# Kernel optimization log

Hardware: AMD Instinct MI355X
Metric: run time of the kernel (lower is better)

Reference implementation:

```python
import jax, jax.numpy as jnp
import numpy as np

N, DIM, H, DH = 2048, 1024, 16, 64
LARGE_NEG = -1e10
LN_EPS = 1e-6  # flax LayerNorm default


def setup_inputs() -> dict:
    key = jax.random.key(0)
    ks = jax.random.split(key, 6)
    x = jax.random.normal(ks[0], (N, DIM), dtype=jnp.float32)
    pos_sin = jax.random.uniform(ks[1], (N - 1, DH // 2), dtype=jnp.float32)
    pos_cos = jax.random.uniform(ks[2], (N - 1, DH // 2), dtype=jnp.float32)
    mask = jax.random.bernoulli(ks[3], 0.9, (N - 1,))
    ln_scale = jnp.ones((DIM,), jnp.float32)
    ln_bias = jnp.zeros((DIM,), jnp.float32)
    w_qkv = jax.random.normal(ks[4], (DIM, 3 * H * DH), jnp.float32) * (DIM ** -0.5)
    w_out = jax.random.normal(ks[5], (H * DH, DIM), jnp.float32) * ((H * DH) ** -0.5)
    b_out = jnp.zeros((DIM,), jnp.float32)
    return {"x": x, "pos_sin": pos_sin, "pos_cos": pos_cos, "mask": mask,
            "ln_scale": ln_scale, "ln_bias": ln_bias,
            "w_qkv": w_qkv, "w_out": w_out, "b_out": b_out}


def _rotate_every_two(t):
    # t: [i, h, d] -> pairwise rotation along d
    x1 = t[:, :, ::2]
    x2 = t[:, :, 1::2]
    return jnp.stack((-x2, x1), axis=-1).reshape(t.shape)


def _apply_rope(t, sin, cos):
    # sin/cos: [i, d/2] -> interleave-repeat to [i, 1, d] (einops 'b n -> b (n j)', j=2)
    sin2 = jnp.repeat(sin, 2, axis=-1)[:, None, :]
    cos2 = jnp.repeat(cos, 2, axis=-1)[:, None, :]
    return t * cos2 + _rotate_every_two(t) * sin2


def reference(x, pos_sin, pos_cos, mask, ln_scale, ln_bias, w_qkv, w_out, b_out):
    n, dim_in = x.shape
    scale = dim_in ** -0.5  # NOTE: full model dim, as in the source

    # LayerNorm over last axis
    mu = jnp.mean(x, axis=-1, keepdims=True)
    var = jnp.mean(jnp.square(x - mu), axis=-1, keepdims=True)
    xn = (x - mu) * jax.lax.rsqrt(var + LN_EPS) * ln_scale + ln_bias

    # QKV projection (no bias)
    qkv = xn @ w_qkv  # [n, 3*h*d]
    q, k, v = jnp.split(qkv, 3, axis=-1)
    q, k, v = (t.reshape(n, H, DH) for t in (q, k, v))

    # Selective RoPE: rotate all positions except the first token
    q = q.at[1:].set(_apply_rope(q[1:], pos_sin, pos_cos))
    k = k.at[1:].set(_apply_rope(k[1:], pos_sin, pos_cos))

    # Head-last similarity [i, j, h]
    sim = jnp.einsum('ihd,jhd->ijh', q, k) * scale

    # Padding mask: prepend True for position 0, broadcast as (1, j, 1)
    pad_mask = jnp.pad(mask, (1, 0), constant_values=True)[None, :, None]

    # Causal mask: triu of an (n-1)x(n-1) block padded with False on row/col 0
    tri = jnp.pad(jnp.ones((n - 1, n - 1), bool), ((1, 0), (1, 0)), constant_values=False)
    causal_mask = jnp.triu(tri, 1)[:, :, None]  # k = j - i + 1 = 1
    full_mask = (~causal_mask) & pad_mask

    sim = jnp.where(full_mask, sim, LARGE_NEG)
    attn = jax.nn.softmax(sim, axis=-2)  # softmax over j (non-last axis)

    out = jnp.einsum('ijh,jhd->ihd', attn, v).reshape(n, H * DH)
    return out @ w_out + b_out
```

## Files before the change

### kernel.cpp

```cpp
#include <hip/hip_runtime.h>
#include <hip/hip_bf16.h>
#include <stdint.h>

typedef __bf16 bf16_t;
typedef __bf16 bf16x8 __attribute__((ext_vector_type(8)));
typedef __bf16 bf16x4 __attribute__((ext_vector_type(4)));
typedef float  f32x4  __attribute__((ext_vector_type(4)));

#define DEV __device__ __forceinline__

static constexpr int NTOK = 2048;
static constexpr int DIM  = 1024;
static constexpr int NH   = 16;
static constexpr int DH   = 64;
static constexpr int QKVN = 3072;
static constexpr int SLOTS_PER_HEAD = 40;
static constexpr int PART_SLOTS = 36;
static constexpr int PART_STRIDE = 17408;
static constexpr float L2E = 1.44269504f;

DEV void gload_lds16(const void* g, void* l) {
  __builtin_amdgcn_global_load_lds(
      (__attribute__((address_space(1))) void*)(g),
      (__attribute__((address_space(3))) void*)(l), 16, 0, 0);
}

DEV float bf2f(bf16_t b) { return (float)b; }

__global__ __launch_bounds__(256) void k_ln_tc(const float* __restrict__ x,
                                               const float* __restrict__ gamma,
                                               const float* __restrict__ beta,
                                               bf16_t* __restrict__ xn,
                                               const float* __restrict__ wsrc,
                                               bf16_t* __restrict__ wdst,
                                               const float* __restrict__ wosrc,
                                               bf16_t* __restrict__ wodst) {
  __shared__ float tile[64][65];
  __shared__ float red[8];
  int b = blockIdx.x;
  if (b < NTOK) {
    const int row = b;
    const int t = threadIdx.x;
    const float4* x4 = reinterpret_cast<const float4*>(x);
    float4 v = x4[(size_t)row * 256 + t];
    float s  = v.x + v.y + v.z + v.w;
    float s2 = v.x * v.x + v.y * v.y + v.z * v.z + v.w * v.w;
#pragma unroll
    for (int o = 1; o < 64; o <<= 1) {
      s  += __shfl_xor(s, o, 64);
      s2 += __shfl_xor(s2, o, 64);
    }
    const int w = t >> 6, lane = t & 63;
    if (lane == 0) { red[w] = s; red[4 + w] = s2; }
    __syncthreads();
    s  = red[0] + red[1] + red[2] + red[3];
    s2 = red[4] + red[5] + red[6] + red[7];
    const float mu  = s * (1.0f / 1024.0f);
    const float var = s2 * (1.0f / 1024.0f) - mu * mu;
    const float inv = rsqrtf(var + 1e-6f);
    const float4 g = reinterpret_cast<const float4*>(gamma)[t];
    const float4 bb = reinterpret_cast<const float4*>(beta)[t];
    bf16x4 o;
    o[0] = (bf16_t)((v.x - mu) * inv * g.x + bb.x);
    o[1] = (bf16_t)((v.y - mu) * inv * g.y + bb.y);
    o[2] = (bf16_t)((v.z - mu) * inv * g.z + bb.z);
    o[3] = (bf16_t)((v.w - mu) * inv * g.w + bb.w);
    *reinterpret_cast<bf16x4*>(xn + (size_t)row * DIM + t * 4) = o;
  } else if (b < NTOK + 768) {
    b -= NTOK;
    const int c0 = (b % 48) * 64;
    const int r0 = (b / 48) * 64;
    const int tx = threadIdx.x & 63;
    const int ty = threadIdx.x >> 6;
#pragma unroll
    for (int i = 0; i < 16; ++i) {
      int r = ty + i * 4;
      tile[r][tx] = wsrc[(size_t)(r0 + r) * 3072 + c0 + tx];
    }
    __syncthreads();
#pragma unroll
    for (int i = 0; i < 16; ++i) {
      int r = ty + i * 4;
      wdst[(size_t)(c0 + r) * 1024 + r0 + tx] = (bf16_t)tile[tx][r];
    }
  } else {
    b -= (NTOK + 768);
    const int c0 = (b & 15) * 64;
    const int r0 = (b >> 4) * 64;
    const int tx = threadIdx.x & 63;
    const int ty = threadIdx.x >> 6;
#pragma unroll
    for (int i = 0; i < 16; ++i) {
      int r = ty + i * 4;
      tile[r][tx] = wosrc[(size_t)(r0 + r) * 1024 + c0 + tx];
    }
    __syncthreads();
#pragma unroll
    for (int i = 0; i < 16; ++i) {
      int r = ty + i * 4;
      wodst[(size_t)(c0 + r) * 1024 + r0 + tx] = (bf16_t)tile[tx][r];
    }
  }
}

__global__ __launch_bounds__(256) void k_gemm_qkv(const bf16_t* __restrict__ A,
                                                  const bf16_t* __restrict__ Bt,
                                                  bf16_t* __restrict__ qkv,
                                                  bf16_t* __restrict__ Vt,
                                                  const float* __restrict__ psin,
                                                  const float* __restrict__ pcos) {
  __shared__ alignas(16) bf16_t As[2][64 * 32];
  __shared__ alignas(16) bf16_t Bs[2][128 * 32];
  const int K = DIM;
  const int tid = threadIdx.x, lane = tid & 63, w = tid >> 6;
  const int bm = blockIdx.x * 64, bn = blockIdx.y * 128;
  const int wr = (w >> 1) * 32, wc = (w & 1) * 64;
  f32x4 acc[2][4];
#pragma unroll
  for (int i = 0; i < 2; ++i)
#pragma unroll
    for (int j = 0; j < 4; ++j) acc[i][j] = f32x4{0.f, 0.f, 0.f, 0.f};

  const int srow  = lane >> 2;
  const int scol8 = (lane & 3) * 8;

#define GSTAGEQ(KT, BUF)                                                              \
  {                                                                                   \
    _Pragma("unroll") for (int it = 0; it < 3; ++it) {                                \
      int s = w * 3 + it;                                                             \
      if (s < 4)                                                                      \
        gload_lds16(A + (size_t)(bm + s * 16 + srow) * K + (KT) + scol8,              \
                    (char*)As + (BUF) * 4096 + s * 1024 + lane * 16);                 \
      else                                                                            \
        gload_lds16(Bt + (size_t)(bn + (s - 4) * 16 + srow) * K + (KT) + scol8,       \
                    (char*)Bs + (BUF) * 8192 + (s - 4) * 1024 + lane * 16);           \
    }                                                                                 \
  }

  GSTAGEQ(0, 0)
  int buf = 0;
  for (int kt = 0; kt < K; kt += 32, buf ^= 1) {
    if (kt + 32 < K) {
      GSTAGEQ(kt + 32, buf ^ 1)
      asm volatile("s_waitcnt vmcnt(3)" ::: "memory");
    } else {
      asm volatile("s_waitcnt vmcnt(0)" ::: "memory");
    }
    __builtin_amdgcn_s_barrier();
    bf16x8 af[2], bfr[4];
#pragma unroll
    for (int i = 0; i < 2; ++i) {
      int mrow = wr + i * 16 + (lane & 15);
      af[i] = *reinterpret_cast<const bf16x8*>((const char*)As + buf * 4096 + mrow * 64 +
                                               (lane >> 4) * 16);
    }
#pragma unroll
    for (int j = 0; j < 4; ++j) {
      int nrow = wc + j * 16 + (lane & 15);
      bfr[j] = *reinterpret_cast<const bf16x8*>((const char*)Bs + buf * 8192 + nrow * 64 +
                                                (lane >> 4) * 16);
    }
#pragma unroll
    for (int i = 0; i < 2; ++i)
#pragma unroll
      for (int j = 0; j < 4; ++j)
        acc[i][j] = __builtin_amdgcn_mfma_f32_16x16x32_bf16(af[i], bfr[j], acc[i][j], 0, 0, 0);
    __builtin_amdgcn_s_barrier();
  }
#undef GSTAGEQ

  if (bn >= 2048) {
#pragma unroll
    for (int i = 0; i < 2; ++i)
#pragma unroll
      for (int j = 0; j < 4; ++j) {
        int d = bn - 2048 + wc + j * 16 + (lane & 15);
        int n0v = bm + wr + i * 16 + (lane >> 4) * 4;
        bf16x4 v4;
#pragma unroll
        for (int r = 0; r < 4; ++r) v4[r] = (bf16_t)acc[i][j][r];
        *reinterpret_cast<bf16x4*>(Vt + (size_t)d * NTOK + n0v) = v4;
      }
  } else {
#pragma unroll
    for (int i = 0; i < 2; ++i)
#pragma unroll
      for (int j = 0; j < 4; ++j) {
        int nn = bn + wc + j * 16 + (lane & 15);
        int tt = (nn & 63) >> 1;
        bool isq = nn < 1024;
#pragma unroll
        for (int r = 0; r < 4; ++r) {
          int mm = bm + wr + i * 16 + (lane >> 4) * 4 + r;
          float v = acc[i][j][r];
          float p = __shfl_xor(v, 1, 64);
          int pidx = (mm >= 1 ? mm - 1 : 0) * 32 + tt;
          float sn = psin[pidx], cs = pcos[pidx];
          float roped = (nn & 1) ? (v * cs + p * sn) : (v * cs - p * sn);
          if (mm < 1) roped = v;
          if (isq && mm >= 1) roped *= 0.03125f;
          qkv[(size_t)mm * QKVN + nn] = (bf16_t)roped;
        }
      }
  }
}

template <int F32OUT>
__global__ __launch_bounds__(256) void k_gemm64(const bf16_t* __restrict__ A,
                                                const bf16_t* __restrict__ Bt,
                                                bf16_t* __restrict__ Cb,
                                                float* __restrict__ Cf,
                                                const float* __restrict__ bias,
                                                int M, int N, int K) {
  __shared__ alignas(16) bf16_t As[2][64 * 32];
  __shared__ alignas(16) bf16_t Bs[2][128 * 32];
  const int tid = threadIdx.x, lane = tid & 63, w = tid >> 6;
  const int bm = blockIdx.x * 64, bn = blockIdx.y * 128;
  const int wr = (w >> 1) * 32, wc = (w & 1) * 64;
  f32x4 acc[2][4];
#pragma unroll
  for (int i = 0; i < 2; ++i)
#pragma unroll
    for (int j = 0; j < 4; ++j) acc[i][j] = f32x4{0.f, 0.f, 0.f, 0.f};

  const int srow  = lane >> 2;
  const int scol8 = (lane & 3) * 8;

#define GSTAGE64(KT, BUF)                                                             \
  {                                                                                   \
    _Pragma("unroll") for (int it = 0; it < 3; ++it) {                                \
      int s = w * 3 + it;                                                             \
      if (s < 4)                                                                      \
        gload_lds16(A + (size_t)(bm + s * 16 + srow) * K + (KT) + scol8,              \
                    (char*)As + (BUF) * 4096 + s * 1024 + lane * 16);                 \
      else                                                                            \
        gload_lds16(Bt + (size_t)(bn + (s - 4) * 16 + srow) * K + (KT) + scol8,       \
                    (char*)Bs + (BUF) * 8192 + (s - 4) * 1024 + lane * 16);           \
    }                                                                                 \
  }

  GSTAGE64(0, 0)
  int buf = 0;
  for (int kt = 0; kt < K; kt += 32, buf ^= 1) {
    if (kt + 32 < K) {
      GSTAGE64(kt + 32, buf ^ 1)
      asm volatile("s_waitcnt vmcnt(3)" ::: "memory");
    } else {
      asm volatile("s_waitcnt vmcnt(0)" ::: "memory");
    }
    __builtin_amdgcn_s_barrier();
    bf16x8 af[2], bfr[4];
#pragma unroll
    for (int i = 0; i < 2; ++i) {
      int mrow = wr + i * 16 + (lane & 15);
      af[i] = *reinterpret_cast<const bf16x8*>((const char*)As + buf * 4096 + mrow * 64 +
                                               (lane >> 4) * 16);
    }
#pragma unroll
    for (int j = 0; j < 4; ++j) {
      int nrow = wc + j * 16 + (lane & 15);
      bfr[j] = *reinterpret_cast<const bf16x8*>((const char*)Bs + buf * 8192 + nrow * 64 +
                                                (lane >> 4) * 16);
    }
#pragma unroll
    for (int i = 0; i < 2; ++i)
#pragma unroll
      for (int j = 0; j < 4; ++j)
        acc[i][j] = __builtin_amdgcn_mfma_f32_16x16x32_bf16(af[i], bfr[j], acc[i][j], 0, 0, 0);
    __builtin_amdgcn_s_barrier();
  }
#undef GSTAGE64

#pragma unroll
  for (int i = 0; i < 2; ++i)
#pragma unroll
    for (int j = 0; j < 4; ++j)
#pragma unroll
      for (int r = 0; r < 4; ++r) {
        int mm = bm + wr + i * 16 + (lane >> 4) * 4 + r;
        int nn = bn + wc + j * 16 + (lane & 15);
        float val = acc[i][j][r];
        if (F32OUT)
          Cf[(size_t)mm * N + nn] = val + bias[nn];
        else
          Cb[(size_t)mm * N + nn] = (bf16_t)val;
      }
}

__global__ __launch_bounds__(512) void k_attn_part(const bf16_t* __restrict__ qkv,
                                                   const bf16_t* __restrict__ Vt,
                                                   const int* __restrict__ mask,
                                                   char* __restrict__ part,
                                                   bf16_t* __restrict__ Ob) {
  __shared__ alignas(16) bf16_t Ks[2][64][64];
  __shared__ alignas(16) bf16_t Vs[2][64][64];
  __shared__ alignas(16) float padf[512];

  const int h = blockIdx.y;

  if (blockIdx.x == SLOTS_PER_HEAD) {
    float* qv   = padf;
    float* sbuf = (float*)Ks;
    float* red  = (float*)Vs;
    float* red2 = (float*)Vs + 64;
    const int t = threadIdx.x, lane = t & 63, w8 = t >> 6;
    if (t < 64) qv[t] = (float)qkv[h * DH + t];
    __syncthreads();
    float sm[4];
    float lmax = -1e30f;
#pragma unroll
    for (int p = 0; p < 4; ++p) {
      int j = p * 512 + t;
      const bf16_t* kr = qkv + (size_t)j * QKVN + DIM + h * DH;
      float s = 0.f;
#pragma unroll
      for (int u = 0; u < 8; ++u) {
        bf16x8 kv8 = *reinterpret_cast<const bf16x8*>(kr + u * 8);
#pragma unroll
        for (int e = 0; e < 8; ++e) s += qv[u * 8 + e] * (float)kv8[e];
      }
      bool padj = (j == 0) || (mask[j - 1] != 0);
      s = padj ? s * 0.03125f : -1e30f;
      sm[p] = s;
      lmax = fmaxf(lmax, s);
    }
#pragma unroll
    for (int o = 1; o < 64; o <<= 1) lmax = fmaxf(lmax, __shfl_xor(lmax, o, 64));
    if (lane == 0) red[w8] = lmax;
    __syncthreads();
    float M = red[0];
#pragma unroll
    for (int i = 1; i < 8; ++i) M = fmaxf(M, red[i]);
    __syncthreads();
    float ls = 0.f;
#pragma unroll
    for (int p = 0; p < 4; ++p) {
      float pe = __expf(sm[p] - M);
      sbuf[p * 512 + t] = pe;
      ls += pe;
    }
#pragma unroll
    for (int o = 1; o < 64; o <<= 1) ls += __shfl_xor(ls, o, 64);
    if (lane == 0) red[w8] = ls;
    __syncthreads();
    float L = red[0];
#pragma unroll
    for (int i = 1; i < 8; ++i) L += red[i];

    const int d = t & 63, qr = t >> 6;
    const bf16_t* vr = Vt + ((size_t)h * DH + d) * NTOK + qr * 256;
    float a = 0.f;
#pragma unroll 8
    for (int u = 0; u < 32; ++u) {
      bf16x8 v8 = *reinterpret_cast<const bf16x8*>(vr + u * 8);
#pragma unroll
      for (int e = 0; e < 8; ++e) a += sbuf[qr * 256 + u * 8 + e] * (float)v8[e];
    }
    red2[qr * 64 + d] = a;
    __syncthreads();
    if (t < 64) {
      float o = 0.f;
#pragma unroll
      for (int i = 0; i < 8; ++i) o += red2[i * 64 + t];
      Ob[h * DH + t] = (bf16_t)(o / L);
    }
    return;
  }

  const int slot = (SLOTS_PER_HEAD - 1) - blockIdx.x;
  int gq;
  if (slot < 4) gq = 0; else if (slot < 12) gq = 1; else if (slot < 24) gq = 2; else gq = 3;
  const int tt = slot - 2 * gq * (gq + 1);
  const int Q = (gq << 2) + tt / (gq + 1);
  const int c2 = tt - (tt / (gq + 1)) * (gq + 1);
  const int q0 = Q * 128;
  const int kbeg = c2 * 512;
  const int kvlen = (Q + 1) * 128;
  const int klen = min(512, kvlen - kbeg);
  const int ntiles = klen >> 6;
  const int nch = gq + 1;

  const int tid = threadIdx.x, lane = tid & 63, w = tid >> 6;
  const int g = lane >> 4;
  const int c = lane & 15;

  for (int jr = tid; jr < klen; jr += 512) {
    int j = kbeg + jr;
    padf[jr] = (j == 0 || mask[j - 1] != 0) ? 1.f : 0.f;
  }

  const int iw = q0 + w * 16;
  bf16x8 qf[2];
  {
    const bf16_t* qp = qkv + (size_t)(iw + c) * QKVN + h * DH + g * 8;
    qf[0] = *reinterpret_cast<const bf16x8*>(qp);
    qf[1] = *reinterpret_cast<const bf16x8*>(qp + 32);
  }
  bf16x8 ones;
#pragma unroll
  for (int e = 0; e < 8; ++e) ones[e] = (bf16_t)1.0f;

  float m_run = -1e30f, m2 = -1e30f;
  f32x4 acc[4], accl;
#pragma unroll
  for (int df = 0; df < 4; ++df) acc[df] = f32x4{0.f, 0.f, 0.f, 0.f};
  accl = f32x4{0.f, 0.f, 0.f, 0.f};

  const int r8 = lane >> 3;

#define STAGE(KB, BUF)                                                                   \
  {                                                                                      \
    _Pragma("unroll") for (int i2 = 0; i2 < 2; ++i2) {                                   \
      int s = w * 2 + i2;                                                                \
      int sw = (lane & 7) ^ r8 ^ ((s & 3) << 1);                                         \
      if (s < 8) {                                                                       \
        int row = s * 8 + r8;                                                            \
        gload_lds16(qkv + (size_t)((KB) + row) * QKVN + DIM + h * DH + sw * 8,           \
                    (char*)Ks + (BUF)*8192 + s * 1024 + lane * 16);                      \
      } else {                                                                           \
        int row = (s - 8) * 8 + r8;                                                      \
        gload_lds16(Vt + ((size_t)h * DH + row) * NTOK + (KB) + sw * 8,                  \
                    (char*)Vs + (BUF)*8192 + (s - 8) * 1024 + lane * 16);                \
      }                                                                                  \
    }                                                                                    \
  }

  STAGE(kbeg, 0)

  for (int it = 0; it < ntiles; ++it) {
    const int buf = it & 1;
    if (it + 1 < ntiles) {
      STAGE(kbeg + (it + 1) * 64, buf ^ 1)
      asm volatile("s_waitcnt vmcnt(2)" ::: "memory");
    } else {
      asm volatile("s_waitcnt vmcnt(0)" ::: "memory");
    }
    __builtin_amdgcn_s_barrier();

    const int k0 = kbeg + it * 64;
    if (k0 <= iw + 15) {
      const char* KsT = (const char*)Ks + buf * 8192;
      const char* VsT = (const char*)Vs + buf * 8192;

      f32x4 sfr[4];
      __builtin_amdgcn_s_setprio(1);
#pragma unroll
      for (int f = 0; f < 4; ++f) {
        int key7 = ((f & 1) * 4) | (c & 3);
        int key = (f >> 1) * 32 + (c >> 2) * 8 + key7;
        int phi = key7 ^ (((c >> 2) & 3) << 1);
        f32x4 s = f32x4{0.f, 0.f, 0.f, 0.f};
#pragma unroll
        for (int kd = 0; kd < 2; ++kd) {
          bf16x8 kf = *reinterpret_cast<const bf16x8*>(
              KsT + key * 128 + (((kd * 4 + g) ^ phi) << 4));
          s = __builtin_amdgcn_mfma_f32_16x16x32_bf16(kf, qf[kd], s, 0, 0, 0);
        }
        sfr[f] = s;
      }
      __builtin_amdgcn_s_setprio(0);

      float pm = fmaxf(fmaxf(sfr[0][0], sfr[0][1]), fmaxf(sfr[0][2], sfr[0][3]));
#pragma unroll
      for (int f = 1; f < 4; ++f)
        pm = fmaxf(pm, fmaxf(fmaxf(sfr[f][0], sfr[f][1]), fmaxf(sfr[f][2], sfr[f][3])));
      pm = fmaxf(pm, __shfl_xor(pm, 16, 64));
      pm = fmaxf(pm, __shfl_xor(pm, 32, 64));

      if (!__all(pm <= m_run + 8.f)) {
        float mnew = fmaxf(m_run, pm);
        float corr = __builtin_amdgcn_exp2f((m_run - mnew) * L2E);
        m_run = mnew;
        m2 = mnew * L2E;
#pragma unroll
        for (int r = 0; r < 4; ++r) {
          float cr = __shfl(corr, g * 4 + r, 64);
          accl[r] *= cr;
#pragma unroll
          for (int df = 0; df < 4; ++df) acc[df][r] *= cr;
        }
      }

      const bool needC = (k0 + 63 > iw);
      const int qlane = iw + c;
      bf16x8 pa[2];
#pragma unroll
      for (int f = 0; f < 4; ++f) {
        int jb = (k0 - kbeg) + (f >> 1) * 32 + g * 8 + (f & 1) * 4;
        f32x4 pad4 = *reinterpret_cast<const f32x4*>(padf + jb);
#pragma unroll
        for (int r = 0; r < 4; ++r) {
          float pe = __builtin_amdgcn_exp2f(__builtin_fmaf(sfr[f][r], L2E, -m2)) * pad4[r];
          if (needC) pe = (kbeg + jb + r <= qlane) ? pe : 0.f;
          pa[f >> 1][(f & 1) * 4 + r] = (bf16_t)pe;
        }
      }

      __builtin_amdgcn_s_setprio(1);
#pragma unroll
      for (int ks = 0; ks < 2; ++ks) {
        accl = __builtin_amdgcn_mfma_f32_16x16x32_bf16(pa[ks], ones, accl, 0, 0, 0);
#pragma unroll
        for (int df = 0; df < 4; ++df) {
          int d = df * 16 + c;
          int phv = (d & 7) ^ (((d >> 3) & 3) << 1);
          bf16x8 vf = *reinterpret_cast<const bf16x8*>(
              VsT + d * 128 + (((ks * 4 + g) ^ phv) << 4));
          acc[df] = __builtin_amdgcn_mfma_f32_16x16x32_bf16(pa[ks], vf, acc[df], 0, 0, 0);
        }
      }
      __builtin_amdgcn_s_setprio(0);
    }
    __builtin_amdgcn_s_barrier();
  }
#undef STAGE

  if (nch == 1) {
#pragma unroll
    for (int r = 0; r < 4; ++r) {
      float inv = 1.0f / accl[r];
      int row = w * 16 + g * 4 + r;
#pragma unroll
      for (int df = 0; df < 4; ++df) {
        if (q0 + row != 0)
          Ob[(size_t)(q0 + row) * DIM + h * DH + df * 16 + c] = (bf16_t)(acc[df][r] * inv);
      }
    }
    return;
  }

  char* pb = part + (size_t)(h * PART_SLOTS + (slot - 4)) * PART_STRIDE;
  bf16_t* po = (bf16_t*)pb;
  float* pmo = (float*)(pb + 16384);
  float* plo = (float*)(pb + 16896);
  float mq[4];
#pragma unroll
  for (int r = 0; r < 4; ++r) mq[r] = __shfl(m2, g * 4 + r, 64);
#pragma unroll
  for (int df = 0; df < 4; ++df)
#pragma unroll
    for (int r = 0; r < 4; ++r) {
      int row = w * 16 + g * 4 + r;
      po[row * 64 + df * 16 + c] = (bf16_t)acc[df][r];
    }
  if (c == 0) {
#pragma unroll
    for (int r = 0; r < 4; ++r) {
      int row = w * 16 + g * 4 + r;
      pmo[row] = mq[r];
      plo[row] = accl[r];
    }
  }
}

__global__ __launch_bounds__(256) void k_merge(const char* __restrict__ part,
                                               bf16_t* __restrict__ Ob) {
  const int Q = blockIdx.x + 4, h = blockIdx.y;
  const int g = Q >> 2, nch = g + 1;
  const int cum = 2 * g * (g + 1) + (Q & 3) * nch - 4;
  const int t = threadIdx.x;
  const int row = t >> 1, half = t & 1;

  float acc[32];
#pragma unroll
  for (int e = 0; e < 32; ++e) acc[e] = 0.f;
  float M = -3e38f, L = 0.f;

  for (int c = 0; c < nch; ++c) {
    const char* pb = part + (size_t)(h * PART_SLOTS + cum + c) * PART_STRIDE;
    float mc = ((const float*)(pb + 16384))[row];
    float lc = ((const float*)(pb + 16896))[row];
    float Mn = fmaxf(M, mc);
    float sOld = __builtin_amdgcn_exp2f(M - Mn), sNew = __builtin_amdgcn_exp2f(mc - Mn);
    M = Mn;
    L = L * sOld + lc * sNew;
    const bf16_t* od = (const bf16_t*)pb + row * 64 + half * 32;
#pragma unroll
    for (int e4 = 0; e4 < 4; ++e4) {
      bf16x8 o8 = *reinterpret_cast<const bf16x8*>(od + e4 * 8);
#pragma unroll
      for (int e = 0; e < 8; ++e)
        acc[e4 * 8 + e] = acc[e4 * 8 + e] * sOld + (float)o8[e] * sNew;
    }
  }
  const float inv = 1.0f / L;
  bf16_t* dst = Ob + (size_t)(Q * 128 + row) * DIM + h * DH + half * 32;
#pragma unroll
  for (int e4 = 0; e4 < 4; ++e4) {
    bf16x8 r8o;
#pragma unroll
    for (int e = 0; e < 8; ++e) r8o[e] = (bf16_t)(acc[e4 * 8 + e] * inv);
    *reinterpret_cast<bf16x8*>(dst + e4 * 8) = r8o;
  }
}

extern "C" void kernel_launch(void* const* d_in, const int* in_sizes, int n_in,
                              void* d_out, int out_size, void* d_ws, size_t ws_size,
                              hipStream_t stream) {
  const float* x       = (const float*)d_in[0];
  const float* pos_sin = (const float*)d_in[1];
  const float* pos_cos = (const float*)d_in[2];
  const int*   mask    = (const int*)d_in[3];
  const float* ln_s    = (const float*)d_in[4];
  const float* ln_b    = (const float*)d_in[5];
  const float* w_qkv   = (const float*)d_in[6];
  const float* w_out   = (const float*)d_in[7];
  const float* b_out   = (const float*)d_in[8];
  float* out = (float*)d_out;

  if (ws_size < 33554432u) return;

  char* ws = (char*)d_ws;
  bf16_t* qkv  = (bf16_t*)(ws + 0);
  bf16_t* Vt   = (bf16_t*)(ws + 12582912);
  bf16_t* Ob   = (bf16_t*)(ws + 16777216);
  bf16_t* Wot  = (bf16_t*)(ws + 20971520);
  bf16_t* xn   = (bf16_t*)(ws + 23068672);
  bf16_t* Wqt  = (bf16_t*)(ws + 27262976);
  char*   part = ws + 23068672;

  k_ln_tc<<<NTOK + 768 + 256, 256, 0, stream>>>(x, ln_s, ln_b, xn, w_qkv, Wqt, w_out, Wot);
  k_gemm_qkv<<<dim3(32, 24), 256, 0, stream>>>(xn, Wqt, qkv, Vt, pos_sin, pos_cos);
  k_attn_part<<<dim3(SLOTS_PER_HEAD + 1, NH), 512, 0, stream>>>(qkv, Vt, mask, part, Ob);
  k_merge<<<dim3(12, 16), 256, 0, stream>>>(part, Ob);
  k_gemm64<1><<<dim3(32, 8), 256, 0, stream>>>(Ob, Wot, nullptr, out, b_out,
                                               NTOK, DIM, DIM);
}
```

Baseline: 96.82 us.

## Enlarge QKV GEMM tile and give each attention wave two query strips

```diff
diff --git a/kernel.cpp b/kernel.cpp
--- a/kernel.cpp
+++ b/kernel.cpp
@@ -109,15 +109,15 @@
                                                   bf16_t* __restrict__ Vt,
                                                   const float* __restrict__ psin,
                                                   const float* __restrict__ pcos) {
-  __shared__ alignas(16) bf16_t As[2][64 * 32];
+  __shared__ alignas(16) bf16_t As[2][128 * 32];
   __shared__ alignas(16) bf16_t Bs[2][128 * 32];
   const int K = DIM;
   const int tid = threadIdx.x, lane = tid & 63, w = tid >> 6;
-  const int bm = blockIdx.x * 64, bn = blockIdx.y * 128;
-  const int wr = (w >> 1) * 32, wc = (w & 1) * 64;
-  f32x4 acc[2][4];
-#pragma unroll
-  for (int i = 0; i < 2; ++i)
+  const int bm = blockIdx.x * 128, bn = blockIdx.y * 128;
+  const int wr = (w >> 1) * 64, wc = (w & 1) * 64;
+  f32x4 acc[4][4];
+#pragma unroll
+  for (int i = 0; i < 4; ++i)
 #pragma unroll
     for (int j = 0; j < 4; ++j) acc[i][j] = f32x4{0.f, 0.f, 0.f, 0.f};
 
@@ -126,14 +126,12 @@
 
 #define GSTAGEQ(KT, BUF)                                                              \
   {                                                                                   \
-    _Pragma("unroll") for (int it = 0; it < 3; ++it) {                                \
-      int s = w * 3 + it;                                                             \
-      if (s < 4)                                                                      \
-        gload_lds16(A + (size_t)(bm + s * 16 + srow) * K + (KT) + scol8,              \
-                    (char*)As + (BUF) * 4096 + s * 1024 + lane * 16);                 \
-      else                                                                            \
-        gload_lds16(Bt + (size_t)(bn + (s - 4) * 16 + srow) * K + (KT) + scol8,       \
-                    (char*)Bs + (BUF) * 8192 + (s - 4) * 1024 + lane * 16);           \
+    _Pragma("unroll") for (int it = 0; it < 2; ++it) {                                \
+      int seg = w * 2 + it;                                                           \
+      gload_lds16(A  + (size_t)(bm + seg * 16 + srow) * K + (KT) + scol8,             \
+                  (char*)As + (BUF) * 8192 + seg * 1024 + lane * 16);                 \
+      gload_lds16(Bt + (size_t)(bn + seg * 16 + srow) * K + (KT) + scol8,             \
+                  (char*)Bs + (BUF) * 8192 + seg * 1024 + lane * 16);                 \
     }                                                                                 \
   }
 
@@ -142,16 +140,16 @@
   for (int kt = 0; kt < K; kt += 32, buf ^= 1) {
     if (kt + 32 < K) {
       GSTAGEQ(kt + 32, buf ^ 1)
-      asm volatile("s_waitcnt vmcnt(3)" ::: "memory");
+      asm volatile("s_waitcnt vmcnt(4)" ::: "memory");
     } else {
       asm volatile("s_waitcnt vmcnt(0)" ::: "memory");
     }
     __builtin_amdgcn_s_barrier();
-    bf16x8 af[2], bfr[4];
-#pragma unroll
-    for (int i = 0; i < 2; ++i) {
+    bf16x8 af[4], bfr[4];
+#pragma unroll
+    for (int i = 0; i < 4; ++i) {
       int mrow = wr + i * 16 + (lane & 15);
-      af[i] = *reinterpret_cast<const bf16x8*>((const char*)As + buf * 4096 + mrow * 64 +
+      af[i] = *reinterpret_cast<const bf16x8*>((const char*)As + buf * 8192 + mrow * 64 +
                                                (lane >> 4) * 16);
     }
 #pragma unroll
@@ -161,7 +159,7 @@
                                                 (lane >> 4) * 16);
     }
 #pragma unroll
-    for (int i = 0; i < 2; ++i)
+    for (int i = 0; i < 4; ++i)
 #pragma unroll
       for (int j = 0; j < 4; ++j)
         acc[i][j] = __builtin_amdgcn_mfma_f32_16x16x32_bf16(af[i], bfr[j], acc[i][j], 0, 0, 0);
@@ -171,7 +169,7 @@
 
   if (bn >= 2048) {
 #pragma unroll
-    for (int i = 0; i < 2; ++i)
+    for (int i = 0; i < 4; ++i)
 #pragma unroll
       for (int j = 0; j < 4; ++j) {
         int d = bn - 2048 + wc + j * 16 + (lane & 15);
@@ -183,7 +181,7 @@
       }
   } else {
 #pragma unroll
-    for (int i = 0; i < 2; ++i)
+    for (int i = 0; i < 4; ++i)
 #pragma unroll
       for (int j = 0; j < 4; ++j) {
         int nn = bn + wc + j * 16 + (lane & 15);
@@ -287,7 +285,7 @@
       }
 }
 
-__global__ __launch_bounds__(512) void k_attn_part(const bf16_t* __restrict__ qkv,
+__global__ __launch_bounds__(256) void k_attn_part(const bf16_t* __restrict__ qkv,
                                                    const bf16_t* __restrict__ Vt,
                                                    const int* __restrict__ mask,
                                                    char* __restrict__ part,
@@ -303,14 +301,14 @@
     float* sbuf = (float*)Ks;
     float* red  = (float*)Vs;
     float* red2 = (float*)Vs + 64;
-    const int t = threadIdx.x, lane = t & 63, w8 = t >> 6;
+    const int t = threadIdx.x, lane = t & 63, w4 = t >> 6;
     if (t < 64) qv[t] = (float)qkv[h * DH + t];
     __syncthreads();
-    float sm[4];
+    float sm[8];
     float lmax = -1e30f;
 #pragma unroll
-    for (int p = 0; p < 4; ++p) {
-      int j = p * 512 + t;
+    for (int p = 0; p < 8; ++p) {
+      int j = p * 256 + t;
       const bf16_t* kr = qkv + (size_t)j * QKVN + DIM + h * DH;
       float s = 0.f;
 #pragma unroll
@@ -326,42 +324,37 @@
     }
 #pragma unroll
     for (int o = 1; o < 64; o <<= 1) lmax = fmaxf(lmax, __shfl_xor(lmax, o, 64));
-    if (lane == 0) red[w8] = lmax;
-    __syncthreads();
-    float M = red[0];
-#pragma unroll
-    for (int i = 1; i < 8; ++i) M = fmaxf(M, red[i]);
+    if (lane == 0) red[w4] = lmax;
+    __syncthreads();
+    const float M = fmaxf(fmaxf(red[0], red[1]), fmaxf(red[2], red[3]));
     __syncthreads();
     float ls = 0.f;
 #pragma unroll
-    for (int p = 0; p < 4; ++p) {
+    for (int p = 0; p < 8; ++p) {
       float pe = __expf(sm[p] - M);
-      sbuf[p * 512 + t] = pe;
+      sbuf[p * 256 + t] = pe;
       ls += pe;
     }
 #pragma unroll
     for (int o = 1; o < 64; o <<= 1) ls += __shfl_xor(ls, o, 64);
-    if (lane == 0) red[w8] = ls;
-    __syncthreads();
-    float L = red[0];
-#pragma unroll
-    for (int i = 1; i < 8; ++i) L += red[i];
+    __syncthreads();
+    if (lane == 0) red[w4] = ls;
+    __syncthreads();
+    const float L = red[0] + red[1] + red[2] + red[3];
 
     const int d = t & 63, qr = t >> 6;
-    const bf16_t* vr = Vt + ((size_t)h * DH + d) * NTOK + qr * 256;
+    const bf16_t* vr = Vt + ((size_t)h * DH + d) * NTOK + qr * 512;
     float a = 0.f;
 #pragma unroll 8
-    for (int u = 0; u < 32; ++u) {
+    for (int u = 0; u < 64; ++u) {
       bf16x8 v8 = *reinterpret_cast<const bf16x8*>(vr + u * 8);
 #pragma unroll
-      for (int e = 0; e < 8; ++e) a += sbuf[qr * 256 + u * 8 + e] * (float)v8[e];
+      for (int e = 0; e < 8; ++e) a += sbuf[qr * 512 + u * 8 + e] * (float)v8[e];
     }
     red2[qr * 64 + d] = a;
     __syncthreads();
     if (t < 64) {
-      float o = 0.f;
-#pragma unroll
-      for (int i = 0; i < 8; ++i) o += red2[i * 64 + t];
+      float o = red2[t] + red2[64 + t] + red2[128 + t] + red2[192 + t];
       Ob[h * DH + t] = (bf16_t)(o / L);
     }
     return;
@@ -384,34 +377,38 @@
   const int g = lane >> 4;
   const int c = lane & 15;
 
-  for (int jr = tid; jr < klen; jr += 512) {
+  for (int jr = tid; jr < klen; jr += 256) {
     int j = kbeg + jr;
     padf[jr] = (j == 0 || mask[j - 1] != 0) ? 1.f : 0.f;
   }
 
-  const int iw = q0 + w * 16;
-  bf16x8 qf[2];
-  {
-    const bf16_t* qp = qkv + (size_t)(iw + c) * QKVN + h * DH + g * 8;
-    qf[0] = *reinterpret_cast<const bf16x8*>(qp);
-    qf[1] = *reinterpret_cast<const bf16x8*>(qp + 32);
+  const int iw = q0 + w * 32;
+  bf16x8 qf[2][2];
+#pragma unroll
+  for (int qh = 0; qh < 2; ++qh) {
+    const bf16_t* qp = qkv + (size_t)(iw + qh * 16 + c) * QKVN + h * DH + g * 8;
+    qf[qh][0] = *reinterpret_cast<const bf16x8*>(qp);
+    qf[qh][1] = *reinterpret_cast<const bf16x8*>(qp + 32);
   }
   bf16x8 ones;
 #pragma unroll
   for (int e = 0; e < 8; ++e) ones[e] = (bf16_t)1.0f;
 
-  float m_run = -1e30f, m2 = -1e30f;
-  f32x4 acc[4], accl;
-#pragma unroll
-  for (int df = 0; df < 4; ++df) acc[df] = f32x4{0.f, 0.f, 0.f, 0.f};
-  accl = f32x4{0.f, 0.f, 0.f, 0.f};
+  float m_run[2] = {-1e30f, -1e30f}, m2_[2] = {-1e30f, -1e30f};
+  f32x4 acc[2][4], accl[2];
+#pragma unroll
+  for (int qh = 0; qh < 2; ++qh) {
+    accl[qh] = f32x4{0.f, 0.f, 0.f, 0.f};
+#pragma unroll
+    for (int df = 0; df < 4; ++df) acc[qh][df] = f32x4{0.f, 0.f, 0.f, 0.f};
+  }
 
   const int r8 = lane >> 3;
 
 #define STAGE(KB, BUF)                                                                   \
   {                                                                                      \
-    _Pragma("unroll") for (int i2 = 0; i2 < 2; ++i2) {                                   \
-      int s = w * 2 + i2;                                                                \
+    _Pragma("unroll") for (int i2 = 0; i2 < 4; ++i2) {                                   \
+      int s = w * 4 + i2;                                                                \
       int sw = (lane & 7) ^ r8 ^ ((s & 3) << 1);                                         \
       if (s < 8) {                                                                       \
         int row = s * 8 + r8;                                                            \
@@ -431,82 +428,104 @@
     const int buf = it & 1;
     if (it + 1 < ntiles) {
       STAGE(kbeg + (it + 1) * 64, buf ^ 1)
-      asm volatile("s_waitcnt vmcnt(2)" ::: "memory");
+      asm volatile("s_waitcnt vmcnt(4)" ::: "memory");
     } else {
       asm volatile("s_waitcnt vmcnt(0)" ::: "memory");
     }
     __builtin_amdgcn_s_barrier();
 
     const int k0 = kbeg + it * 64;
-    if (k0 <= iw + 15) {
+    if (k0 <= iw + 31) {
       const char* KsT = (const char*)Ks + buf * 8192;
       const char* VsT = (const char*)Vs + buf * 8192;
 
-      f32x4 sfr[4];
+      f32x4 sfr[2][4];
       __builtin_amdgcn_s_setprio(1);
 #pragma unroll
       for (int f = 0; f < 4; ++f) {
         int key7 = ((f & 1) * 4) | (c & 3);
         int key = (f >> 1) * 32 + (c >> 2) * 8 + key7;
         int phi = key7 ^ (((c >> 2) & 3) << 1);
-        f32x4 s = f32x4{0.f, 0.f, 0.f, 0.f};
+        f32x4 s0 = f32x4{0.f, 0.f, 0.f, 0.f};
+        f32x4 s1 = f32x4{0.f, 0.f, 0.f, 0.f};
 #pragma unroll
         for (int kd = 0; kd < 2; ++kd) {
           bf16x8 kf = *reinterpret_cast<const bf16x8*>(
               KsT + key * 128 + (((kd * 4 + g) ^ phi) << 4));
-          s = __builtin_amdgcn_mfma_f32_16x16x32_bf16(kf, qf[kd], s, 0, 0, 0);
+          s0 = __builtin_amdgcn_mfma_f32_16x16x32_bf16(kf, qf[0][kd], s0, 0, 0, 0);
+          s1 = __builtin_amdgcn_mfma_f32_16x16x32_bf16(kf, qf[1][kd], s1, 0, 0, 0);
         }
-        sfr[f] = s;
+        sfr[0][f] = s0;
+        sfr[1][f] = s1;
       }
       __builtin_amdgcn_s_setprio(0);
 
-      float pm = fmaxf(fmaxf(sfr[0][0], sfr[0][1]), fmaxf(sfr[0][2], sfr[0][3]));
-#pragma unroll
-      for (int f = 1; f < 4; ++f)
-        pm = fmaxf(pm, fmaxf(fmaxf(sfr[f][0], sfr[f][1]), fmaxf(sfr[f][2], sfr[f][3])));
-      pm = fmaxf(pm, __shfl_xor(pm, 16, 64));
-      pm = fmaxf(pm, __shfl_xor(pm, 32, 64));
-
-      if (!__all(pm <= m_run + 8.f)) {
-        float mnew = fmaxf(m_run, pm);
-        float corr = __builtin_amdgcn_exp2f((m_run - mnew) * L2E);
-        m_run = mnew;
-        m2 = mnew * L2E;
-#pragma unroll
-        for (int r = 0; r < 4; ++r) {
-          float cr = __shfl(corr, g * 4 + r, 64);
-          accl[r] *= cr;
-#pragma unroll
-          for (int df = 0; df < 4; ++df) acc[df][r] *= cr;
+      float pm[2];
+#pragma unroll
+      for (int qh = 0; qh < 2; ++qh) {
+        float p = fmaxf(fmaxf(sfr[qh][0][0], sfr[qh][0][1]),
+                        fmaxf(sfr[qh][0][2], sfr[qh][0][3]));
+#pragma unroll
+        for (int f = 1; f < 4; ++f)
+          p = fmaxf(p, fmaxf(fmaxf(sfr[qh][f][0], sfr[qh][f][1]),
+                             fmaxf(sfr[qh][f][2], sfr[qh][f][3])));
+        p = fmaxf(p, __shfl_xor(p, 16, 64));
+        p = fmaxf(p, __shfl_xor(p, 32, 64));
+        pm[qh] = p;
+      }
+
+      int dok = (pm[0] <= m_run[0] + 8.f) && (pm[1] <= m_run[1] + 8.f);
+      if (!__all(dok)) {
+#pragma unroll
+        for (int qh = 0; qh < 2; ++qh) {
+          float mnew = fmaxf(m_run[qh], pm[qh]);
+          float corr = __builtin_amdgcn_exp2f((m_run[qh] - mnew) * L2E);
+          m_run[qh] = mnew;
+          m2_[qh] = mnew * L2E;
+#pragma unroll
+          for (int r = 0; r < 4; ++r) {
+            float cr = __shfl(corr, g * 4 + r, 64);
+            accl[qh][r] *= cr;
+#pragma unroll
+            for (int df = 0; df < 4; ++df) acc[qh][df][r] *= cr;
+          }
         }
       }
 
-      const bool needC = (k0 + 63 > iw);
-      const int qlane = iw + c;
-      bf16x8 pa[2];
-#pragma unroll
-      for (int f = 0; f < 4; ++f) {
-        int jb = (k0 - kbeg) + (f >> 1) * 32 + g * 8 + (f & 1) * 4;
-        f32x4 pad4 = *reinterpret_cast<const f32x4*>(padf + jb);
-#pragma unroll
-        for (int r = 0; r < 4; ++r) {
-          float pe = __builtin_amdgcn_exp2f(__builtin_fmaf(sfr[f][r], L2E, -m2)) * pad4[r];
-          if (needC) pe = (kbeg + jb + r <= qlane) ? pe : 0.f;
-          pa[f >> 1][(f & 1) * 4 + r] = (bf16_t)pe;
+      bf16x8 pa[2][2];
+#pragma unroll
+      for (int qh = 0; qh < 2; ++qh) {
+        const bool needC = (k0 + 63 > iw + qh * 16);
+        const int qlane = iw + qh * 16 + c;
+#pragma unroll
+        for (int f = 0; f < 4; ++f) {
+          int jb = (k0 - kbeg) + (f >> 1) * 32 + g * 8 + (f & 1) * 4;
+          f32x4 pad4 = *reinterpret_cast<const f32x4*>(padf + jb);
+#pragma unroll
+          for (int r = 0; r < 4; ++r) {
+            float pe = __builtin_amdgcn_exp2f(__builtin_fmaf(sfr[qh][f][r], L2E, -m2_[qh])) *
+                       pad4[r];
+            if (needC) pe = (kbeg + jb + r <= qlane) ? pe : 0.f;
+            pa[qh][f >> 1][(f & 1) * 4 + r] = (bf16_t)pe;
+          }
         }
       }
 
       __builtin_amdgcn_s_setprio(1);
 #pragma unroll
       for (int ks = 0; ks < 2; ++ks) {
-        accl = __builtin_amdgcn_mfma_f32_16x16x32_bf16(pa[ks], ones, accl, 0, 0, 0);
+        accl[0] = __builtin_amdgcn_mfma_f32_16x16x32_bf16(pa[0][ks], ones, accl[0], 0, 0, 0);
+        accl[1] = __builtin_amdgcn_mfma_f32_16x16x32_bf16(pa[1][ks], ones, accl[1], 0, 0, 0);
 #pragma unroll
         for (int df = 0; df < 4; ++df) {
           int d = df * 16 + c;
           int phv = (d & 7) ^ (((d >> 3) & 3) << 1);
           bf16x8 vf = *reinterpret_cast<const bf16x8*>(
               VsT + d * 128 + (((ks * 4 + g) ^ phv) << 4));
-          acc[df] = __builtin_amdgcn_mfma_f32_16x16x32_bf16(pa[ks], vf, acc[df], 0, 0, 0);
+          acc[0][df] = __builtin_amdgcn_mfma_f32_16x16x32_bf16(pa[0][ks], vf, acc[0][df],
+                                                               0, 0, 0);
+          acc[1][df] = __builtin_amdgcn_mfma_f32_16x16x32_bf16(pa[1][ks], vf, acc[1][df],
+                                                               0, 0, 0);
         }
       }
       __builtin_amdgcn_s_setprio(0);
@@ -517,15 +536,18 @@
 
   if (nch == 1) {
 #pragma unroll
-    for (int r = 0; r < 4; ++r) {
-      float inv = 1.0f / accl[r];
-      int row = w * 16 + g * 4 + r;
-#pragma unroll
-      for (int df = 0; df < 4; ++df) {
-        if (q0 + row != 0)
-          Ob[(size_t)(q0 + row) * DIM + h * DH + df * 16 + c] = (bf16_t)(acc[df][r] * inv);
-      }
-    }
+    for (int qh = 0; qh < 2; ++qh)
+#pragma unroll
+      for (int r = 0; r < 4; ++r) {
+        float inv = 1.0f / accl[qh][r];
+        int row = w * 32 + qh * 16 + g * 4 + r;
+#pragma unroll
+        for (int df = 0; df < 4; ++df) {
+          if (q0 + row != 0)
+            Ob[(size_t)(q0 + row) * DIM + h * DH + df * 16 + c] =
+                (bf16_t)(acc[qh][df][r] * inv);
+        }
+      }
     return;
   }
 
@@ -533,22 +555,22 @@
   bf16_t* po = (bf16_t*)pb;
   float* pmo = (float*)(pb + 16384);
   float* plo = (float*)(pb + 16896);
-  float mq[4];
-#pragma unroll
-  for (int r = 0; r < 4; ++r) mq[r] = __shfl(m2, g * 4 + r, 64);
-#pragma unroll
-  for (int df = 0; df < 4; ++df)
-#pragma unroll
-    for (int r = 0; r < 4; ++r) {
-      int row = w * 16 + g * 4 + r;
-      po[row * 64 + df * 16 + c] = (bf16_t)acc[df][r];
-    }
-  if (c == 0) {
-#pragma unroll
-    for (int r = 0; r < 4; ++r) {
-      int row = w * 16 + g * 4 + r;
-      pmo[row] = mq[r];
-      plo[row] = accl[r];
+#pragma unroll
+  for (int qh = 0; qh < 2; ++qh) {
+#pragma unroll
+    for (int df = 0; df < 4; ++df)
+#pragma unroll
+      for (int r = 0; r < 4; ++r) {
+        int row = w * 32 + qh * 16 + g * 4 + r;
+        po[row * 64 + df * 16 + c] = (bf16_t)acc[qh][df][r];
+      }
+    if (c == 0) {
+#pragma unroll
+      for (int r = 0; r < 4; ++r) {
+        int row = w * 32 + qh * 16 + g * 4 + r;
+        pmo[row] = __shfl(m2_[qh], g * 4 + r, 64);
+        plo[row] = accl[qh][r];
+      }
     }
   }
 }
@@ -620,8 +642,8 @@
   char*   part = ws + 23068672;
 
   k_ln_tc<<<NTOK + 768 + 256, 256, 0, stream>>>(x, ln_s, ln_b, xn, w_qkv, Wqt, w_out, Wot);
-  k_gemm_qkv<<<dim3(32, 24), 256, 0, stream>>>(xn, Wqt, qkv, Vt, pos_sin, pos_cos);
-  k_attn_part<<<dim3(SLOTS_PER_HEAD + 1, NH), 512, 0, stream>>>(qkv, Vt, mask, part, Ob);
+  k_gemm_qkv<<<dim3(16, 24), 256, 0, stream>>>(xn, Wqt, qkv, Vt, pos_sin, pos_cos);
+  k_attn_part<<<dim3(SLOTS_PER_HEAD + 1, NH), 256, 0, stream>>>(qkv, Vt, mask, part, Ob);
   k_merge<<<dim3(12, 16), 256, 0, stream>>>(part, Ob);
   k_gemm64<1><<<dim3(32, 8), 256, 0, stream>>>(Ob, Wot, nullptr, out, b_out,
                                                NTOK, DIM, DIM);
```

Result: slower. 104.8 us (+8.2%).
